# Performance work log

Hardware: AMD Instinct MI355X
Metric: run time of the kernel (lower is better)

Reference implementation:

```python
import jax, jax.numpy as jnp
import numpy as np

N_NODES = 50000
N_EDGES = 800000
D_IN = 512
D_OUT = 256

def setup_inputs() -> dict:
    key = jax.random.key(0)
    k1, k2, k3, k4, k5 = jax.random.split(key, 5)
    return {
        "inputs": jax.random.normal(k1, (N_NODES, D_IN), dtype=jnp.float32),
        "weights": jax.random.uniform(k2, (D_IN, D_OUT), dtype=jnp.float32, minval=-0.1, maxval=0.1),
        "bias": jnp.zeros((D_OUT,), dtype=jnp.float32),
        "edge_vals": jax.random.uniform(k3, (N_EDGES,), dtype=jnp.float32),
        "edge_row": jax.random.randint(k4, (N_EDGES,), 0, N_NODES),
        "edge_col": jax.random.randint(k5, (N_EDGES,), 0, N_NODES),
    }

def reference(inputs, weights, bias, edge_vals, edge_row, edge_col):
    # dense projection: [N, D_in] @ [D_in, D_out] -> [N, D_out]
    supports = inputs @ weights
    # sparse adjacency spmm in COO form: out[i] = sum_e vals[e] * supports[col[e]] for row[e] == i
    msgs = supports[edge_col] * edge_vals[:, None]  # [E, D_out]
    aggregated = jax.ops.segment_sum(msgs, edge_row, num_segments=inputs.shape[0])
    return aggregated + bias
```

## Files before the change

### kernel.cpp

```cpp
#include <hip/hip_runtime.h>

#define D_IN 512
#define D_OUT 256
#define BM 64
#define BN 256
#define BK 64

typedef short short8 __attribute__((ext_vector_type(8)));
typedef float floatx4 __attribute__((ext_vector_type(4)));

static __device__ __forceinline__ unsigned short f2bf(float f) {
    unsigned u = __float_as_uint(f);
    u += 0x7FFF + ((u >> 16) & 1);
    return (unsigned short)(u >> 16);
}
static __device__ __forceinline__ float bf2f(unsigned short h) {
    return __uint_as_float((unsigned)h << 16);
}

#define CONV_BLOCKS 256
__global__ __launch_bounds__(512) void convert_and_zero(const float* __restrict__ W,
                                                        unsigned short* __restrict__ Wt,
                                                        int* __restrict__ cnt, int M) {
    int b = blockIdx.x;
    if (b < CONV_BLOCKS) {
        int t = b * 512 + threadIdx.x;
        int n = t >> 9;
        int k = t & 511;
        Wt[t] = f2bf(W[(size_t)k * D_OUT + n]);
    } else {
        int i = (b - CONV_BLOCKS) * 512 + threadIdx.x;
        if (i < M) cnt[i] = 0;
    }
}

__global__ __launch_bounds__(256) void hist_rows(const int* __restrict__ rows,
                                                 int* __restrict__ cnt, int E) {
    int e0 = (blockIdx.x * 256 + threadIdx.x) * 4;
    if (e0 + 3 < E) {
        int4 r = *(const int4*)(rows + e0);
        atomicAdd(&cnt[r.x], 1);
        atomicAdd(&cnt[r.y], 1);
        atomicAdd(&cnt[r.z], 1);
        atomicAdd(&cnt[r.w], 1);
    } else {
        for (int e = e0; e < E; ++e) atomicAdd(&cnt[rows[e]], 1);
    }
}

#define SCAN_B 4096
__global__ __launch_bounds__(1024) void scan_blocks(const int* __restrict__ cnt,
                                                    int* __restrict__ ptr,
                                                    int* __restrict__ partials, int M) {
    __shared__ int wsum[16];
    const int t = threadIdx.x, lane = t & 63, wave = t >> 6;
    const int base = blockIdx.x * SCAN_B + t * 4;
    int4 v = make_int4(0, 0, 0, 0);
    if (base + 3 < M) v = *(const int4*)(cnt + base);
    else {
        if (base + 0 < M) v.x = cnt[base + 0];
        if (base + 1 < M) v.y = cnt[base + 1];
        if (base + 2 < M) v.z = cnt[base + 2];
        if (base + 3 < M) v.w = cnt[base + 3];
    }
    int s = v.x + v.y + v.z + v.w;
    int incl = s;
#pragma unroll
    for (int off = 1; off < 64; off <<= 1) {
        int x = __shfl_up(incl, off, 64);
        if (lane >= off) incl += x;
    }
    if (lane == 63) wsum[wave] = incl;
    __syncthreads();
    if (t == 0) {
        int run = 0;
#pragma unroll
        for (int w = 0; w < 16; ++w) { int x = wsum[w]; wsum[w] = run; run += x; }
        partials[blockIdx.x] = run;
    }
    __syncthreads();
    int e0 = wsum[wave] + (incl - s);
    int e1 = e0 + v.x, e2 = e1 + v.y, e3 = e2 + v.z;
    if (base + 3 < M) *(int4*)(ptr + base) = make_int4(e0, e1, e2, e3);
    else {
        if (base + 0 < M) ptr[base + 0] = e0;
        if (base + 1 < M) ptr[base + 1] = e1;
        if (base + 2 < M) ptr[base + 2] = e2;
        if (base + 3 < M) ptr[base + 3] = e3;
    }
}

__global__ __launch_bounds__(256) void add_offsets(int* __restrict__ ptr,
                                                   const int* __restrict__ partials,
                                                   int M) {
    int i = blockIdx.x * 256 + threadIdx.x;
    if (i >= M) return;
    int bucket = blockIdx.x >> 4;
    int off = 0;
    for (int j = 0; j < bucket; ++j) off += partials[j];
    ptr[i] += off;
}

__global__ __launch_bounds__(512, 4) void gemm_build(
    const float* __restrict__ A, const unsigned short* __restrict__ Wt,
    unsigned short* __restrict__ S, int M, int nBuild,
    const float* __restrict__ vals, const int* __restrict__ rows,
    const int* __restrict__ cols, int* __restrict__ ptr,
    unsigned long long* __restrict__ edges, int E) {
    __shared__ unsigned short As[(BK / 8) * BM * 8];
    __shared__ unsigned short Bs[(BK / 8) * BN * 8];
    const int bid = blockIdx.x;
    const int tid = threadIdx.x;

    if (bid < nBuild) {
        int e0 = bid * 2048 + tid * 4;
        if (e0 + 3 < E) {
            int4   rr = *(const int4*)(rows + e0);
            int4   cc = *(const int4*)(cols + e0);
            float4 vv = *(const float4*)(vals + e0);
            int p0 = atomicAdd(&ptr[rr.x], 1);
            __builtin_nontemporal_store(
                (unsigned long long)(unsigned)cc.x |
                ((unsigned long long)(unsigned)__float_as_int(vv.x) << 32), edges + p0);
            int p1 = atomicAdd(&ptr[rr.y], 1);
            __builtin_nontemporal_store(
                (unsigned long long)(unsigned)cc.y |
                ((unsigned long long)(unsigned)__float_as_int(vv.y) << 32), edges + p1);
            int p2 = atomicAdd(&ptr[rr.z], 1);
            __builtin_nontemporal_store(
                (unsigned long long)(unsigned)cc.z |
                ((unsigned long long)(unsigned)__float_as_int(vv.z) << 32), edges + p2);
            int p3 = atomicAdd(&ptr[rr.w], 1);
            __builtin_nontemporal_store(
                (unsigned long long)(unsigned)cc.w |
                ((unsigned long long)(unsigned)__float_as_int(vv.w) << 32), edges + p3);
        } else {
            for (int e = e0; e < E; ++e) {
                int pos = atomicAdd(&ptr[rows[e]], 1);
                unsigned long long packed =
                    (unsigned long long)(unsigned)cols[e] |
                    ((unsigned long long)(unsigned)__float_as_int(vals[e]) << 32);
                __builtin_nontemporal_store(packed, edges + pos);
            }
        }
        return;
    }

    const int gi   = bid - nBuild;
    const int bm   = gi * BM;
    const int lane = tid & 63;
    const int wave = tid >> 6;
    const int l15  = lane & 15;
    const int quad = lane >> 4;
    const int wn   = wave * 32;

    const int ar = (wave & 3) * 16 + l15;
    const int ap = (wave >> 2) * 4 + quad;
    const bool aval = (bm + ar) < M;
    const float* aptr = A + (size_t)(aval ? bm + ar : 0) * D_IN + ap * 8;
    const int asoff = (ap * BM + ar) * 8;

    const int bn_ = tid >> 1;
    const int bh  = tid & 1;
    const unsigned short* bptr = Wt + (size_t)bn_ * D_IN + bh * 32;

    float4 aR0 = aval ? *(const float4*)(aptr + 0) : make_float4(0.f, 0.f, 0.f, 0.f);
    float4 aR1 = aval ? *(const float4*)(aptr + 4) : make_float4(0.f, 0.f, 0.f, 0.f);
    short8 bR[4];
#pragma unroll
    for (int j = 0; j < 4; ++j) bR[j] = *(const short8*)(bptr + 8 * j);

    floatx4 acc[4][2] = {};

    for (int k0 = 0; k0 < D_IN; k0 += BK) {
        short8 a8;
        a8[0] = (short)f2bf(aR0.x); a8[1] = (short)f2bf(aR0.y);
        a8[2] = (short)f2bf(aR0.z); a8[3] = (short)f2bf(aR0.w);
        a8[4] = (short)f2bf(aR1.x); a8[5] = (short)f2bf(aR1.y);
        a8[6] = (short)f2bf(aR1.z); a8[7] = (short)f2bf(aR1.w);
        *(short8*)(As + asoff) = a8;
#pragma unroll
        for (int j = 0; j < 4; ++j)
            *(short8*)(Bs + ((bh * 4 + j) * BN + bn_) * 8) = bR[j];
        __syncthreads();

        if (k0 + BK < D_IN) {
            aR0 = aval ? *(const float4*)(aptr + k0 + BK + 0) : make_float4(0.f, 0.f, 0.f, 0.f);
            aR1 = aval ? *(const float4*)(aptr + k0 + BK + 4) : make_float4(0.f, 0.f, 0.f, 0.f);
#pragma unroll
            for (int j = 0; j < 4; ++j)
                bR[j] = *(const short8*)(bptr + k0 + BK + 8 * j);
        }

#pragma unroll
        for (int s = 0; s < 2; ++s) {
            const int p = s * 4 + quad;
            short8 af[4], bfr[2];
#pragma unroll
            for (int i = 0; i < 4; ++i)
                af[i] = *(const short8*)(As + (p * BM + i * 16 + l15) * 8);
#pragma unroll
            for (int j = 0; j < 2; ++j)
                bfr[j] = *(const short8*)(Bs + (p * BN + wn + j * 16 + l15) * 8);
#pragma unroll
            for (int i = 0; i < 4; ++i)
#pragma unroll
                for (int j = 0; j < 2; ++j)
                    acc[i][j] = __builtin_amdgcn_mfma_f32_16x16x32_bf16(
                        af[i], bfr[j], acc[i][j], 0, 0, 0);
        }
        __syncthreads();
    }

#pragma unroll
    for (int i = 0; i < 4; ++i) {
#pragma unroll
        for (int r = 0; r < 4; ++r) {
            int gm = bm + i * 16 + quad * 4 + r;
            if (gm < M) {
#pragma unroll
                for (int j = 0; j < 2; ++j)
                    S[(size_t)gm * D_OUT + wn + j * 16 + l15] = f2bf(acc[i][j][r]);
            }
        }
    }
}

__global__ __launch_bounds__(256) void spmm_rows(const unsigned short* __restrict__ S,
                                                 const int2* __restrict__ edges,
                                                 const int* __restrict__ ptr,
                                                 const float* __restrict__ bias,
                                                 float* __restrict__ out, int M) {
    const int row = blockIdx.x * 4 + (threadIdx.x >> 6);
    if (row >= M) return;
    const int lane = threadIdx.x & 63;
    float4 a0 = ((const float4*)bias)[lane];
    float4 a1 = make_float4(0.f, 0.f, 0.f, 0.f);
    const int beg = row ? ptr[row - 1] : 0;
    const int end = ptr[row];
    int j = beg;
    for (; j + 7 < end; j += 8) {
        int2 e0 = edges[j + 0], e1 = edges[j + 1], e2 = edges[j + 2], e3 = edges[j + 3];
        int2 e4 = edges[j + 4], e5 = edges[j + 5], e6 = edges[j + 6], e7 = edges[j + 7];
        ushort4 s0 = ((const ushort4*)(S + (size_t)e0.x * D_OUT))[lane];
        ushort4 s1 = ((const ushort4*)(S + (size_t)e1.x * D_OUT))[lane];
        ushort4 s2 = ((const ushort4*)(S + (size_t)e2.x * D_OUT))[lane];
        ushort4 s3 = ((const ushort4*)(S + (size_t)e3.x * D_OUT))[lane];
        ushort4 s4 = ((const ushort4*)(S + (size_t)e4.x * D_OUT))[lane];
        ushort4 s5 = ((const ushort4*)(S + (size_t)e5.x * D_OUT))[lane];
        ushort4 s6 = ((const ushort4*)(S + (size_t)e6.x * D_OUT))[lane];
        ushort4 s7 = ((const ushort4*)(S + (size_t)e7.x * D_OUT))[lane];
        float v0 = __int_as_float(e0.y), v1 = __int_as_float(e1.y);
        float v2 = __int_as_float(e2.y), v3 = __int_as_float(e3.y);
        float v4 = __int_as_float(e4.y), v5 = __int_as_float(e5.y);
        float v6 = __int_as_float(e6.y), v7 = __int_as_float(e7.y);
        a0.x += v0 * bf2f(s0.x) + v2 * bf2f(s2.x) + v4 * bf2f(s4.x) + v6 * bf2f(s6.x);
        a0.y += v0 * bf2f(s0.y) + v2 * bf2f(s2.y) + v4 * bf2f(s4.y) + v6 * bf2f(s6.y);
        a0.z += v0 * bf2f(s0.z) + v2 * bf2f(s2.z) + v4 * bf2f(s4.z) + v6 * bf2f(s6.z);
        a0.w += v0 * bf2f(s0.w) + v2 * bf2f(s2.w) + v4 * bf2f(s4.w) + v6 * bf2f(s6.w);
        a1.x += v1 * bf2f(s1.x) + v3 * bf2f(s3.x) + v5 * bf2f(s5.x) + v7 * bf2f(s7.x);
        a1.y += v1 * bf2f(s1.y) + v3 * bf2f(s3.y) + v5 * bf2f(s5.y) + v7 * bf2f(s7.y);
        a1.z += v1 * bf2f(s1.z) + v3 * bf2f(s3.z) + v5 * bf2f(s5.z) + v7 * bf2f(s7.z);
        a1.w += v1 * bf2f(s1.w) + v3 * bf2f(s3.w) + v5 * bf2f(s5.w) + v7 * bf2f(s7.w);
    }
    for (; j + 3 < end; j += 4) {
        int2 e0 = edges[j], e1 = edges[j + 1], e2 = edges[j + 2], e3 = edges[j + 3];
        ushort4 s0 = ((const ushort4*)(S + (size_t)e0.x * D_OUT))[lane];
        ushort4 s1 = ((const ushort4*)(S + (size_t)e1.x * D_OUT))[lane];
        ushort4 s2 = ((const ushort4*)(S + (size_t)e2.x * D_OUT))[lane];
        ushort4 s3 = ((const ushort4*)(S + (size_t)e3.x * D_OUT))[lane];
        float v0 = __int_as_float(e0.y), v1 = __int_as_float(e1.y);
        float v2 = __int_as_float(e2.y), v3 = __int_as_float(e3.y);
        a0.x += v0 * bf2f(s0.x) + v2 * bf2f(s2.x);
        a0.y += v0 * bf2f(s0.y) + v2 * bf2f(s2.y);
        a0.z += v0 * bf2f(s0.z) + v2 * bf2f(s2.z);
        a0.w += v0 * bf2f(s0.w) + v2 * bf2f(s2.w);
        a1.x += v1 * bf2f(s1.x) + v3 * bf2f(s3.x);
        a1.y += v1 * bf2f(s1.y) + v3 * bf2f(s3.y);
        a1.z += v1 * bf2f(s1.z) + v3 * bf2f(s3.z);
        a1.w += v1 * bf2f(s1.w) + v3 * bf2f(s3.w);
    }
    for (; j < end; ++j) {
        int2 e = edges[j];
        float v = __int_as_float(e.y);
        ushort4 s = ((const ushort4*)(S + (size_t)e.x * D_OUT))[lane];
        a0.x += v * bf2f(s.x);
        a0.y += v * bf2f(s.y);
        a0.z += v * bf2f(s.z);
        a0.w += v * bf2f(s.w);
    }
    a0.x += a1.x; a0.y += a1.y; a0.z += a1.z; a0.w += a1.w;
    floatx4 res = {a0.x, a0.y, a0.z, a0.w};
    __builtin_nontemporal_store(res, (floatx4*)(out + (size_t)row * D_OUT) + lane);
}

extern "C" void kernel_launch(void* const* d_in, const int* in_sizes, int n_in,
                              void* d_out, int out_size, void* d_ws, size_t ws_size,
                              hipStream_t stream) {
    const float* inputs    = (const float*)d_in[0];
    const float* weights   = (const float*)d_in[1];
    const float* bias      = (const float*)d_in[2];
    const float* edge_vals = (const float*)d_in[3];
    const int*   edge_row  = (const int*)d_in[4];
    const int*   edge_col  = (const int*)d_in[5];
    float* out = (float*)d_out;

    const int M = in_sizes[0] / D_IN;
    const int E = in_sizes[3];

    char* ws = (char*)d_ws;
    unsigned short* S  = (unsigned short*)ws;
    unsigned short* Wt = (unsigned short*)(ws + (size_t)M * D_OUT * 2);
    unsigned long long* edges = (unsigned long long*)((char*)Wt + (size_t)D_OUT * D_IN * 2);
    int*  ptr          = (int*)((char*)edges + (size_t)E * 8);
    int*  cnt          = ptr + ((M + 4) & ~3);
    int*  partials     = cnt + M;

    int nzero = (M + 511) / 512;
    convert_and_zero<<<CONV_BLOCKS + nzero, 512, 0, stream>>>(weights, Wt, cnt, M);

    hist_rows<<<(E + 1023) / 1024, 256, 0, stream>>>(edge_row, cnt, E);
    int nb = (M + SCAN_B - 1) / SCAN_B;
    scan_blocks<<<nb, 1024, 0, stream>>>(cnt, ptr, partials, M);
    add_offsets<<<(M + 255) / 256, 256, 0, stream>>>(ptr, partials, M);

    int nGemm  = (M + BM - 1) / BM;
    int nBuild = (E + 2047) / 2048;
    gemm_build<<<nBuild + nGemm, 512, 0, stream>>>(inputs, Wt, S, M, nBuild,
                                                   edge_vals, edge_row, edge_col,
                                                   ptr, edges, E);

    spmm_rows<<<(M + 3) / 4, 256, 0, stream>>>(S, (const int2*)edges, ptr, bias, out, M);
}
```

Before: 333.6 us.

## Fuse scan offset pass via decoupled lookback, double-buffer GEMM K-loop, reorder blocks

```diff
diff --git a/kernel.cpp b/kernel.cpp
--- a/kernel.cpp
+++ b/kernel.cpp
@@ -4,7 +4,8 @@
 #define D_OUT 256
 #define BM 64
 #define BN 256
-#define BK 64
+#define BK 32
+#define NT (D_IN / BK)
 
 typedef short short8 __attribute__((ext_vector_type(8)));
 typedef float floatx4 __attribute__((ext_vector_type(4)));
@@ -21,7 +22,7 @@
 #define CONV_BLOCKS 256
 __global__ __launch_bounds__(512) void convert_and_zero(const float* __restrict__ W,
                                                         unsigned short* __restrict__ Wt,
-                                                        int* __restrict__ cnt, int M) {
+                                                        int* __restrict__ cnt, int NZ) {
     int b = blockIdx.x;
     if (b < CONV_BLOCKS) {
         int t = b * 512 + threadIdx.x;
@@ -30,7 +31,7 @@
         Wt[t] = f2bf(W[(size_t)k * D_OUT + n]);
     } else {
         int i = (b - CONV_BLOCKS) * 512 + threadIdx.x;
-        if (i < M) cnt[i] = 0;
+        if (i < NZ) cnt[i] = 0;
     }
 }
 
@@ -49,10 +50,12 @@
 }
 
 #define SCAN_B 4096
+#define SCAN_READY (1 << 30)
 __global__ __launch_bounds__(1024) void scan_blocks(const int* __restrict__ cnt,
                                                     int* __restrict__ ptr,
                                                     int* __restrict__ partials, int M) {
     __shared__ int wsum[16];
+    __shared__ int s_off;
     const int t = threadIdx.x, lane = t & 63, wave = t >> 6;
     const int base = blockIdx.x * SCAN_B + t * 4;
     int4 v = make_int4(0, 0, 0, 0);
@@ -76,11 +79,18 @@
         int run = 0;
 #pragma unroll
         for (int w = 0; w < 16; ++w) { int x = wsum[w]; wsum[w] = run; run += x; }
-        partials[blockIdx.x] = run;
+        atomicExch(&partials[blockIdx.x], run | SCAN_READY);
+        int off = 0;
+        for (int j = 0; j < (int)blockIdx.x; ++j) {
+            int pv;
+            do { pv = atomicAdd(&partials[j], 0); } while (!(pv & SCAN_READY));
+            off += pv & ~SCAN_READY;
+        }
+        s_off = off;
     }
     __syncthreads();
-    int e0 = wsum[wave] + (incl - s);
-    int e1 = e0 + v.x, e2 = e1 + v.y, e3 = e2 + v.z;
+    int g = s_off + wsum[wave] + (incl - s);
+    int e0 = g, e1 = e0 + v.x, e2 = e1 + v.y, e3 = e2 + v.z;
     if (base + 3 < M) *(int4*)(ptr + base) = make_int4(e0, e1, e2, e3);
     else {
         if (base + 0 < M) ptr[base + 0] = e0;
@@ -90,30 +100,19 @@
     }
 }
 
-__global__ __launch_bounds__(256) void add_offsets(int* __restrict__ ptr,
-                                                   const int* __restrict__ partials,
-                                                   int M) {
-    int i = blockIdx.x * 256 + threadIdx.x;
-    if (i >= M) return;
-    int bucket = blockIdx.x >> 4;
-    int off = 0;
-    for (int j = 0; j < bucket; ++j) off += partials[j];
-    ptr[i] += off;
-}
-
-__global__ __launch_bounds__(512, 4) void gemm_build(
+__global__ __launch_bounds__(512) void gemm_build(
     const float* __restrict__ A, const unsigned short* __restrict__ Wt,
-    unsigned short* __restrict__ S, int M, int nBuild,
+    unsigned short* __restrict__ S, int M, int nGemm,
     const float* __restrict__ vals, const int* __restrict__ rows,
     const int* __restrict__ cols, int* __restrict__ ptr,
     unsigned long long* __restrict__ edges, int E) {
-    __shared__ unsigned short As[(BK / 8) * BM * 8];
-    __shared__ unsigned short Bs[(BK / 8) * BN * 8];
+    __shared__ unsigned short As[4 * BM * 8];
+    __shared__ unsigned short Bs[4 * BN * 8];
     const int bid = blockIdx.x;
     const int tid = threadIdx.x;
 
-    if (bid < nBuild) {
-        int e0 = bid * 2048 + tid * 4;
+    if (bid >= nGemm) {
+        int e0 = (bid - nGemm) * 2048 + tid * 4;
         if (e0 + 3 < E) {
             int4   rr = *(const int4*)(rows + e0);
             int4   cc = *(const int4*)(cols + e0);
@@ -146,71 +145,83 @@
         return;
     }
 
-    const int gi   = bid - nBuild;
-    const int bm   = gi * BM;
+    const int bm   = bid * BM;
     const int lane = tid & 63;
     const int wave = tid >> 6;
     const int l15  = lane & 15;
     const int quad = lane >> 4;
     const int wn   = wave * 32;
 
-    const int ar = (wave & 3) * 16 + l15;
-    const int ap = (wave >> 2) * 4 + quad;
-    const bool aval = (bm + ar) < M;
-    const float* aptr = A + (size_t)(aval ? bm + ar : 0) * D_IN + ap * 8;
-    const int asoff = (ap * BM + ar) * 8;
-
-    const int bn_ = tid >> 1;
-    const int bh  = tid & 1;
-    const unsigned short* bptr = Wt + (size_t)bn_ * D_IN + bh * 32;
-
-    float4 aR0 = aval ? *(const float4*)(aptr + 0) : make_float4(0.f, 0.f, 0.f, 0.f);
-    float4 aR1 = aval ? *(const float4*)(aptr + 4) : make_float4(0.f, 0.f, 0.f, 0.f);
-    short8 bR[4];
-#pragma unroll
-    for (int j = 0; j < 4; ++j) bR[j] = *(const short8*)(bptr + 8 * j);
+    const bool isA  = tid < 256;
+    const int  arow = tid & 63;
+    const int  apl  = (tid >> 6) & 3;
+    const bool aval = isA && (bm + arow) < M;
+    const float* aptr = A + (size_t)(aval ? bm + arow : 0) * D_IN + apl * 8;
+    const int awoff = (apl * BM + arow) * 8;
+
+    const int brow = tid & 255;
+    const int bp0  = tid >> 8;
+    const unsigned short* bptr0 = Wt + (size_t)brow * D_IN + bp0 * 8;
+    const unsigned short* bptr1 = Wt + (size_t)brow * D_IN + (bp0 + 2) * 8;
+    const int bwoff0 = (bp0 * BN + brow) * 8;
+    const int bwoff1 = ((bp0 + 2) * BN + brow) * 8;
+
+    float4 a0lo, a0hi, a1lo, a1hi;
+    short8 b0r0, b0r1, b1r0, b1r1;
+    const float4 fz = make_float4(0.f, 0.f, 0.f, 0.f);
+    a0lo = aval ? *(const float4*)(aptr + 0) : fz;
+    a0hi = aval ? *(const float4*)(aptr + 4) : fz;
+    b0r0 = *(const short8*)(bptr0 + 0);
+    b0r1 = *(const short8*)(bptr1 + 0);
+    a1lo = aval ? *(const float4*)(aptr + BK) : fz;
+    a1hi = aval ? *(const float4*)(aptr + BK + 4) : fz;
+    b1r0 = *(const short8*)(bptr0 + BK);
+    b1r1 = *(const short8*)(bptr1 + BK);
 
     floatx4 acc[4][2] = {};
 
-    for (int k0 = 0; k0 < D_IN; k0 += BK) {
-        short8 a8;
-        a8[0] = (short)f2bf(aR0.x); a8[1] = (short)f2bf(aR0.y);
-        a8[2] = (short)f2bf(aR0.z); a8[3] = (short)f2bf(aR0.w);
-        a8[4] = (short)f2bf(aR1.x); a8[5] = (short)f2bf(aR1.y);
-        a8[6] = (short)f2bf(aR1.z); a8[7] = (short)f2bf(aR1.w);
-        *(short8*)(As + asoff) = a8;
-#pragma unroll
-        for (int j = 0; j < 4; ++j)
-            *(short8*)(Bs + ((bh * 4 + j) * BN + bn_) * 8) = bR[j];
-        __syncthreads();
-
-        if (k0 + BK < D_IN) {
-            aR0 = aval ? *(const float4*)(aptr + k0 + BK + 0) : make_float4(0.f, 0.f, 0.f, 0.f);
-            aR1 = aval ? *(const float4*)(aptr + k0 + BK + 4) : make_float4(0.f, 0.f, 0.f, 0.f);
-#pragma unroll
-            for (int j = 0; j < 4; ++j)
-                bR[j] = *(const short8*)(bptr + k0 + BK + 8 * j);
-        }
-
-#pragma unroll
-        for (int s = 0; s < 2; ++s) {
-            const int p = s * 4 + quad;
-            short8 af[4], bfr[2];
-#pragma unroll
-            for (int i = 0; i < 4; ++i)
-                af[i] = *(const short8*)(As + (p * BM + i * 16 + l15) * 8);
-#pragma unroll
-            for (int j = 0; j < 2; ++j)
-                bfr[j] = *(const short8*)(Bs + (p * BN + wn + j * 16 + l15) * 8);
-#pragma unroll
-            for (int i = 0; i < 4; ++i)
-#pragma unroll
-                for (int j = 0; j < 2; ++j)
-                    acc[i][j] = __builtin_amdgcn_mfma_f32_16x16x32_bf16(
-                        af[i], bfr[j], acc[i][j], 0, 0, 0);
-        }
-        __syncthreads();
-    }
+#define GEMM_STEP(T, ALO, AHI, BR0, BR1)                                          \
+    {                                                                             \
+        if (isA) {                                                                \
+            short8 a8;                                                            \
+            a8[0] = (short)f2bf(ALO.x); a8[1] = (short)f2bf(ALO.y);               \
+            a8[2] = (short)f2bf(ALO.z); a8[3] = (short)f2bf(ALO.w);               \
+            a8[4] = (short)f2bf(AHI.x); a8[5] = (short)f2bf(AHI.y);               \
+            a8[6] = (short)f2bf(AHI.z); a8[7] = (short)f2bf(AHI.w);               \
+            *(short8*)(As + awoff) = a8;                                          \
+        }                                                                         \
+        *(short8*)(Bs + bwoff0) = BR0;                                            \
+        *(short8*)(Bs + bwoff1) = BR1;                                            \
+        __syncthreads();                                                          \
+        if ((T) + 2 < NT) {                                                       \
+            int ko = ((T) + 2) * BK;                                              \
+            ALO = aval ? *(const float4*)(aptr + ko) : fz;                        \
+            AHI = aval ? *(const float4*)(aptr + ko + 4) : fz;                    \
+            BR0 = *(const short8*)(bptr0 + ko);                                   \
+            BR1 = *(const short8*)(bptr1 + ko);                                   \
+        }                                                                         \
+        short8 af[4], bfr[2];                                                     \
+        _Pragma("unroll")                                                         \
+        for (int i = 0; i < 4; ++i)                                               \
+            af[i] = *(const short8*)(As + (quad * BM + i * 16 + l15) * 8);        \
+        _Pragma("unroll")                                                         \
+        for (int j = 0; j < 2; ++j)                                               \
+            bfr[j] = *(const short8*)(Bs + (quad * BN + wn + j * 16 + l15) * 8);  \
+        _Pragma("unroll")                                                         \
+        for (int i = 0; i < 4; ++i)                                               \
+            _Pragma("unroll")                                                     \
+            for (int j = 0; j < 2; ++j)                                           \
+                acc[i][j] = __builtin_amdgcn_mfma_f32_16x16x32_bf16(              \
+                    af[i], bfr[j], acc[i][j], 0, 0, 0);                           \
+        __syncthreads();                                                          \
+    }
+
+#pragma unroll
+    for (int t2 = 0; t2 < NT; t2 += 2) {
+        GEMM_STEP(t2,     a0lo, a0hi, b0r0, b0r1);
+        GEMM_STEP(t2 + 1, a1lo, a1hi, b1r0, b1r1);
+    }
+#undef GEMM_STEP
 
 #pragma unroll
     for (int i = 0; i < 4; ++i) {
@@ -316,17 +327,15 @@
     int*  cnt          = ptr + ((M + 4) & ~3);
     int*  partials     = cnt + M;
 
-    int nzero = (M + 511) / 512;
-    convert_and_zero<<<CONV_BLOCKS + nzero, 512, 0, stream>>>(weights, Wt, cnt, M);
+    int NZ = M + 16;
+    convert_and_zero<<<CONV_BLOCKS + (NZ + 511) / 512, 512, 0, stream>>>(weights, Wt, cnt, NZ);
 
     hist_rows<<<(E + 1023) / 1024, 256, 0, stream>>>(edge_row, cnt, E);
-    int nb = (M + SCAN_B - 1) / SCAN_B;
-    scan_blocks<<<nb, 1024, 0, stream>>>(cnt, ptr, partials, M);
-    add_offsets<<<(M + 255) / 256, 256, 0, stream>>>(ptr, partials, M);
+    scan_blocks<<<(M + SCAN_B - 1) / SCAN_B, 1024, 0, stream>>>(cnt, ptr, partials, M);
 
     int nGemm  = (M + BM - 1) / BM;
     int nBuild = (E + 2047) / 2048;
-    gemm_build<<<nBuild + nGemm, 512, 0, stream>>>(inputs, Wt, S, M, nBuild,
+    gemm_build<<<nGemm + nBuild, 512, 0, stream>>>(inputs, Wt, S, M, nGemm,
                                                    edge_vals, edge_row, edge_col,
                                                    ptr, edges, E);
 
```

Result: slower. 360.4 us (+8.0%).
